# Kernel tuning notes

Measured on AMD Instinct MI355X. Metric: run time of the kernel, lower is better.

## Reference

```python
import jax, jax.numpy as jnp
import numpy as np

B, T, R = 512, 4096, 16


def setup_inputs() -> dict:
    key = jax.random.key(0)
    k1, k2, k3 = jax.random.split(key, 3)
    pred = jax.random.normal(k1, (B, T, R), dtype=jnp.float32)
    target = jax.random.normal(k2, (B, T, R), dtype=jnp.float32)
    # replicate_mask marks a contiguous prefix of valid replicates (matches
    # the original `pred[b, :, :n_valid]` slicing). Lengths in [0, R].
    lengths = jax.random.randint(k3, (B,), 0, R + 1)
    replicate_mask = (jnp.arange(R)[None, :] < lengths[:, None]).astype(jnp.float32)
    return {"pred": pred, "target": target, "replicate_mask": replicate_mask}


def _masked_var_unbiased(x, m, n_safe):
    # x: [B,T,R], m: [B,1,R], n_safe: [B,1] (clamped >= 2)
    mean = jnp.sum(x * m, axis=-1, keepdims=True) / n_safe[:, :, None]  # [B,T,1]
    sq = jnp.sum(((x - mean) ** 2) * m, axis=-1)  # [B,T]
    return sq / (n_safe - 1.0)  # unbiased (torch var default ddof=1)


def reference(pred, target, replicate_mask):
    weight = 0.1
    n = jnp.sum(replicate_mask, axis=-1)  # [B]
    n_safe = jnp.maximum(n, 2.0)[:, None]  # avoid div-by-zero; masked out below
    m = replicate_mask[:, None, :]  # [B,1,R]
    pred_var = _masked_var_unbiased(pred, m, n_safe)      # [B,T]
    target_var = _masked_var_unbiased(target, m, n_safe)  # [B,T]
    mse = jnp.mean((pred_var - target_var) ** 2, axis=-1)  # [B]
    valid = n > 1.0
    n_multi = jnp.sum(valid.astype(jnp.float32))
    total = jnp.sum(jnp.where(valid, mse, 0.0))
    loss = jnp.where(n_multi > 0, total / jnp.maximum(n_multi, 1.0), 0.0)
    return weight * loss
```

## Files before the change

kernel.cpp:

```cpp
#include <hip/hip_runtime.h>

#define B_DIM 512
#define T_DIM 4096
#define NSLOT 256
#define BLOCKS 4096
#define THREADS 256
#define ITER 8

__device__ __forceinline__ float hsum4(float4 v) { return (v.x + v.y) + (v.z + v.w); }

__device__ __forceinline__ float mdot(float4 x, float4 m) {
    return (x.x * m.x + x.y * m.y) + (x.z * m.z + x.w * m.w);
}

__device__ __forceinline__ float mdot2(float4 x, float4 m) {
    return (x.x * x.x * m.x + x.y * x.y * m.y) + (x.z * x.z * m.z + x.w * x.w * m.w);
}

__device__ __forceinline__ float qsum(float v) {
    int t = __builtin_amdgcn_update_dpp(0, __float_as_int(v), 0xB1, 0xF, 0xF, true);
    v += __int_as_float(t);
    t = __builtin_amdgcn_update_dpp(0, __float_as_int(v), 0x4E, 0xF, 0xF, true);
    v += __int_as_float(t);
    return v;
}

__global__ __launch_bounds__(THREADS) void rcl_main(
    const float4* __restrict__ pred4, const float4* __restrict__ targ4,
    const float4* __restrict__ mask4, double* __restrict__ slots)
{
    const int tid0 = blockIdx.x * THREADS + threadIdx.x;

    float4 mv[ITER], pv[ITER], qv[ITER];
#pragma unroll
    for (int i = 0; i < ITER; i++) {
        const int g = tid0 + i * (BLOCKS * THREADS);
        pv[i] = pred4[g];
        qv[i] = targ4[g];
        mv[i] = mask4[((g >> 14) << 2) + (g & 3)];
    }

    float csum = 0.0f;
#pragma unroll
    for (int i = 0; i < ITER; i++) {
        const float4 m = mv[i], p = pv[i], q = qv[i];
        float n   = qsum(hsum4(m));
        float sp  = qsum(mdot(p, m));
        float sp2 = qsum(mdot2(p, m));
        float sq  = qsum(mdot(q, m));
        float sq2 = qsum(mdot2(q, m));

        float nsafe = fmaxf(n, 2.0f);
        float inv = 1.0f / (nsafe * (nsafe - 1.0f));
        float d = ((nsafe * sp2 - sp * sp) - (nsafe * sq2 - sq * sq)) * inv;
        csum += (n > 1.0f) ? d * d * 0.25f : 0.0f;
    }

    for (int off = 32; off > 0; off >>= 1)
        csum += __shfl_down(csum, off, 64);

    __shared__ float partial[THREADS / 64];
    const int lane = threadIdx.x & 63;
    const int w = threadIdx.x >> 6;
    if (lane == 0) partial[w] = csum;
    __syncthreads();
    if (threadIdx.x == 0) {
        float s = (partial[0] + partial[1]) + (partial[2] + partial[3]);
        atomicAdd(&slots[blockIdx.x & (NSLOT - 1)], (double)s);
    }
}

__global__ __launch_bounds__(256) void rcl_final(
    const double* __restrict__ slots, const float4* __restrict__ mask4,
    float* __restrict__ out)
{
    __shared__ double dred[256];
    __shared__ float fred[256];
    const int t = threadIdx.x;

    double tot = slots[t];

    float cnt = 0.0f;
    for (int bb = t; bb < B_DIM; bb += 256) {
        const float4* mp = mask4 + (bb << 2);
        float nn = (hsum4(mp[0]) + hsum4(mp[1])) + (hsum4(mp[2]) + hsum4(mp[3]));
        cnt += (nn > 1.0f) ? 1.0f : 0.0f;
    }

    dred[t] = tot;
    fred[t] = cnt;
    __syncthreads();
    for (int s = 128; s > 0; s >>= 1) {
        if (t < s) { dred[t] += dred[t + s]; fred[t] += fred[t + s]; }
        __syncthreads();
    }
    if (t == 0) {
        double nm = (double)fred[0];
        out[0] = (nm > 0.0) ? (float)(0.1 * (dred[0] / ((double)T_DIM * nm))) : 0.0f;
    }
}

extern "C" void kernel_launch(void* const* d_in, const int* in_sizes, int n_in,
                              void* d_out, int out_size, void* d_ws, size_t ws_size,
                              hipStream_t stream) {
    const float4* pred4 = (const float4*)d_in[0];
    const float4* targ4 = (const float4*)d_in[1];
    const float4* mask4 = (const float4*)d_in[2];
    float* out = (float*)d_out;

    double* slots = (double*)d_ws;

    hipMemsetAsync(d_ws, 0, NSLOT * sizeof(double), stream);
    rcl_main<<<BLOCKS, THREADS, 0, stream>>>(pred4, targ4, mask4, slots);
    rcl_final<<<1, 256, 0, stream>>>(slots, mask4, out);
}
```

Before: 290.5 us.

## Skip loading rows with fewer than two replicates and stage loads via LDS DMA

Computes each row's replicate count from the mask first, and only fetches pred and target rows whose count exceeds one. Those rows are fetched with asynchronous global-to-LDS loads into a shared buffer and read back after a barrier. The grid grows to more blocks with fewer rows per thread. This cuts HBM traffic for rows that contribute nothing to the loss, in exchange for LDS round-trips, an extra barrier, and reliance on the barrier correctly waiting for the LDS DMA writes.

Result: faster. 267.9 us (-7.8%).

```diff
diff --git a/kernel.cpp b/kernel.cpp
--- a/kernel.cpp
+++ b/kernel.cpp
@@ -3,9 +3,10 @@
 #define B_DIM 512
 #define T_DIM 4096
 #define NSLOT 256
-#define BLOCKS 4096
+#define BLOCKS 16384
 #define THREADS 256
-#define ITER 8
+#define NWAVE (THREADS / 64)
+#define ITER 2
 
 __device__ __forceinline__ float hsum4(float4 v) { return (v.x + v.y) + (v.z + v.w); }
 
@@ -25,46 +26,68 @@
     return v;
 }
 
+__device__ __forceinline__ void stage16(const float4* g, float4* l) {
+    __builtin_amdgcn_global_load_lds((const __attribute__((address_space(1))) void*)g,
+                                     (__attribute__((address_space(3))) void*)l, 16, 0, 0);
+}
+
 __global__ __launch_bounds__(THREADS) void rcl_main(
     const float4* __restrict__ pred4, const float4* __restrict__ targ4,
     const float4* __restrict__ mask4, double* __restrict__ slots)
 {
-    const int tid0 = blockIdx.x * THREADS + threadIdx.x;
+    __shared__ float4 buf[2][NWAVE][ITER][64];
 
-    float4 mv[ITER], pv[ITER], qv[ITER];
+    const int tid = threadIdx.x;
+    const int w = tid >> 6;
+    const int lane = tid & 63;
+    const int tid0 = blockIdx.x * THREADS + tid;
+
+    float4 mv[ITER];
 #pragma unroll
     for (int i = 0; i < ITER; i++) {
         const int g = tid0 + i * (BLOCKS * THREADS);
-        pv[i] = pred4[g];
-        qv[i] = targ4[g];
         mv[i] = mask4[((g >> 14) << 2) + (g & 3)];
     }
+
+    float nval[ITER];
+#pragma unroll
+    for (int i = 0; i < ITER; i++) {
+        const int g = tid0 + i * (BLOCKS * THREADS);
+        nval[i] = qsum(hsum4(mv[i]));
+        if (nval[i] > 1.0f) {
+            stage16(&pred4[g], &buf[0][w][i][0]);
+            stage16(&targ4[g], &buf[1][w][i][0]);
+        }
+    }
+
+    __syncthreads();
 
     float csum = 0.0f;
 #pragma unroll
     for (int i = 0; i < ITER; i++) {
-        const float4 m = mv[i], p = pv[i], q = qv[i];
-        float n   = qsum(hsum4(m));
-        float sp  = qsum(mdot(p, m));
-        float sp2 = qsum(mdot2(p, m));
-        float sq  = qsum(mdot(q, m));
-        float sq2 = qsum(mdot2(q, m));
+        if (nval[i] > 1.0f) {
+            const float4 m = mv[i];
+            const float4 p = buf[0][w][i][lane];
+            const float4 q = buf[1][w][i][lane];
+            float sp  = qsum(mdot(p, m));
+            float sp2 = qsum(mdot2(p, m));
+            float sq  = qsum(mdot(q, m));
+            float sq2 = qsum(mdot2(q, m));
 
-        float nsafe = fmaxf(n, 2.0f);
-        float inv = 1.0f / (nsafe * (nsafe - 1.0f));
-        float d = ((nsafe * sp2 - sp * sp) - (nsafe * sq2 - sq * sq)) * inv;
-        csum += (n > 1.0f) ? d * d * 0.25f : 0.0f;
+            const float n = nval[i];
+            float inv = 1.0f / (n * (n - 1.0f));
+            float d = ((n * sp2 - sp * sp) - (n * sq2 - sq * sq)) * inv;
+            csum += d * d * 0.25f;
+        }
     }
 
     for (int off = 32; off > 0; off >>= 1)
         csum += __shfl_down(csum, off, 64);
 
-    __shared__ float partial[THREADS / 64];
-    const int lane = threadIdx.x & 63;
-    const int w = threadIdx.x >> 6;
+    __shared__ float partial[NWAVE];
     if (lane == 0) partial[w] = csum;
     __syncthreads();
-    if (threadIdx.x == 0) {
+    if (tid == 0) {
         float s = (partial[0] + partial[1]) + (partial[2] + partial[3]);
         atomicAdd(&slots[blockIdx.x & (NSLOT - 1)], (double)s);
     }
```
